# Kernel tuning notes

Hardware: AMD Instinct MI355X
Metric: run time of the kernel (lower is better)

## Reference

```python
import jax, jax.numpy as jnp
import numpy as np

N_SITES = 64   # lattice sites
BOND = 32      # virtual bond dimension D
PHYS = 2       # physical (spin) dimension
BATCH = 32768  # Monte Carlo samples


def spin_to_occupancy(s):
    # spins in {-1,+1} -> physical indices in {0,1}
    return ((s + 1) // 2).astype(jnp.int32)


def setup_inputs() -> dict:
    key = jax.random.key(0)
    k1, k2, k3, k4 = jax.random.split(key, 4)
    # site tensors: boundary sites have bond dim 1, interior sites are (PHYS, D, D)
    t_first = jax.random.uniform(k1, (PHYS, 1, BOND), dtype=jnp.float32)
    t_mid = jax.random.uniform(k2, (N_SITES - 2, PHYS, BOND, BOND), dtype=jnp.float32)
    t_last = jax.random.uniform(k3, (PHYS, BOND, 1), dtype=jnp.float32)
    bits = jax.random.randint(k4, (BATCH, N_SITES), 0, 2)
    x = (2 * bits - 1).astype(jnp.int32)  # spins +-1
    return {"t_first": t_first, "t_mid": t_mid, "t_last": t_last, "x": x}


def reference(t_first, t_mid, t_last, x):
    idx = spin_to_occupancy(x)  # (B, n_sites)
    # first site: left bond = 1, so state = t_first[idx0, 0, :]  (B, D)
    state = t_first[idx[:, 0], 0, :]

    # interior sites: sequential chain of gather + batched mat-vec
    def step(state, xs):
        T, i = xs            # T: (PHYS, D, D), i: (B,)
        mats = T[i]          # (B, D, D) gather by physical index
        return jnp.einsum('bi,bij->bj', state, mats), None

    state, _ = jax.lax.scan(step, state, (t_mid, idx[:, 1:-1].T))

    # last site: right bond = 1
    amps = jnp.einsum('bi,bi->b', state, t_last[idx[:, -1], :, 0])  # (B,)
    return jnp.log(amps)
```

## Files before the change

kernel.cpp:

```cpp
#include <hip/hip_runtime.h>
#include <math.h>

#define N_MID 62
#define NPAIR 31
#define BATCH 32768

typedef float f32x4 __attribute__((ext_vector_type(4)));
typedef unsigned int u32x2 __attribute__((ext_vector_type(2)));
typedef unsigned int u32x4 __attribute__((ext_vector_type(4)));

__device__ __forceinline__ long mklong(unsigned a, unsigned b) {
    u32x2 t = {a, b};
    return __builtin_bit_cast(long, t);
}
__device__ __forceinline__ unsigned pack_fp8x4(float a, float b, float c, float d) {
    int r = __builtin_amdgcn_cvt_pk_fp8_f32(a, b, 0, false);
    r = __builtin_amdgcn_cvt_pk_fp8_f32(c, d, r, true);
    return (unsigned)r;
}

__global__ __launch_bounds__(64) void prefix_kernel(const float* __restrict__ t_mid,
                                                    unsigned* __restrict__ wsP) {
    __shared__ float M1s[1024], M2s[1024];
    const int l = threadIdx.x, q = l >> 4, m = l & 15;
    const int i = blockIdx.x >> 2, v = blockIdx.x & 3;

    const float4* s1 = (const float4*)(t_mid + (size_t)((2 * i) * 2 + (v & 1)) * 1024);
    const float4* s2 = (const float4*)(t_mid + (size_t)((2 * i + 1) * 2 + (v >> 1)) * 1024);
    #pragma unroll
    for (int c = 0; c < 4; ++c) {
        ((float4*)M1s)[c * 64 + l] = s1[c * 64 + l];
        ((float4*)M2s)[c * 64 + l] = s2[c * 64 + l];
    }
    __syncthreads();

    float colv[2][32];
    #pragma unroll
    for (int t = 0; t < 2; ++t)
        #pragma unroll
        for (int mm = 0; mm < 32; ++mm)
            colv[t][mm] = M2s[mm * 32 + 16 * t + m];

    float o0[8], o1[8];
    #pragma unroll
    for (int j = 0; j < 8; ++j) {
        int a = 16 * (j >> 2) + 4 * q + (j & 3);
        float acc0 = 0.f, acc1 = 0.f;
        #pragma unroll
        for (int mm = 0; mm < 32; ++mm) {
            float r = M1s[a * 32 + mm];
            acc0 = fmaf(r, colv[0][mm], acc0);
            acc1 = fmaf(r, colv[1][mm], acc1);
        }
        o0[j] = acc0;
        o1[j] = acc1;
    }

    u32x4 outw;
    outw[0] = pack_fp8x4(o0[0], o0[1], o0[2], o0[3]);
    outw[1] = pack_fp8x4(o0[4], o0[5], o0[6], o0[7]);
    outw[2] = pack_fp8x4(o1[0], o1[1], o1[2], o1[3]);
    outw[3] = pack_fp8x4(o1[4], o1[5], o1[6], o1[7]);
    ((u32x4*)wsP)[blockIdx.x * 64 + l] = outw;
}

__global__ __launch_bounds__(256, 2) void mps_mfma_kernel(
    const float* __restrict__ t_first,
    const float* __restrict__ t_last,
    const int*   __restrict__ x,
    const unsigned* __restrict__ wsP,
    float* __restrict__ out)
{
    const int tid  = threadIdx.x;
    const int w    = tid >> 6;
    const int l    = tid & 63;
    const int q    = l >> 4;
    const int e    = l & 15;
    const int base = (blockIdx.x * 4 + w) * 16;

    unsigned long long mrot;
    {
        const int4* xr = (const int4*)(x + (size_t)(base + e) * 64 + 16 * q);
        unsigned chunk = 0;
        #pragma unroll
        for (int c = 0; c < 4; ++c) {
            int4 vv = xr[c];
            chunk |= (unsigned)(vv.x > 0) << (4 * c + 0);
            chunk |= (unsigned)(vv.y > 0) << (4 * c + 1);
            chunk |= (unsigned)(vv.z > 0) << (4 * c + 2);
            chunk |= (unsigned)(vv.w > 0) << (4 * c + 3);
        }
        unsigned sh = chunk << ((q & 1) * 16);
        unsigned lo = (q < 2) ? sh : 0u;
        unsigned hi = (q >= 2) ? sh : 0u;
        lo |= (unsigned)__shfl_xor((int)lo, 16);
        lo |= (unsigned)__shfl_xor((int)lo, 32);
        hi |= (unsigned)__shfl_xor((int)hi, 16);
        hi |= (unsigned)__shfl_xor((int)hi, 32);
        unsigned long long mask = ((unsigned long long)hi << 32) | lo;
        const float* tf = t_first + ((mask & 1ull) ? 32 : 0);
        mrot = mask >> 1;
        (void)tf;
    }

    float st[8];
    {
        const float* tf = t_first + ((x[(size_t)(base + e) * 64] > 0) ? 32 : 0);
        #pragma unroll
        for (int j = 0; j < 8; ++j)
            st[j] = tf[16 * (j >> 2) + 4 * q + (j & 3)];
    }
    unsigned Bd0 = pack_fp8x4(st[0], st[1], st[2], st[3]);
    unsigned Bd1 = pack_fp8x4(st[4], st[5], st[6], st[7]);

    int expsum = 0;
    const f32x4 cz = {0.f, 0.f, 0.f, 0.f};

    const u32x4* W = (const u32x4*)wsP + l;
    u32x4 Q0[4], Q1[4];
    #pragma unroll
    for (int v = 0; v < 4; ++v) Q0[v] = W[v * 64];
    #pragma unroll
    for (int v = 0; v < 4; ++v) Q1[v] = W[(4 + v) * 64];

    auto step = [&](u32x4* Q, const u32x4* pf) {
        unsigned vl = (unsigned)mrot & 3u;
        mrot >>= 2;

        f32x4 y0 = cz, y1 = cz;
        #pragma unroll
        for (int v = 0; v < 4; ++v) {
            long A0 = mklong(Q[v][0], Q[v][1]);
            long A1 = mklong(Q[v][2], Q[v][3]);
            bool sel = (vl == (unsigned)v);
            long u = mklong(sel ? Bd0 : 0u, sel ? Bd1 : 0u);
            y0 = __builtin_amdgcn_mfma_f32_16x16x32_fp8_fp8(A0, u, y0, 0, 0, 0);
            y1 = __builtin_amdgcn_mfma_f32_16x16x32_fp8_fp8(A1, u, y1, 0, 0, 0);
        }

        if (pf) {
            #pragma unroll
            for (int v = 0; v < 4; ++v) Q[v] = pf[v * 64];
        }

        #pragma unroll
        for (int r = 0; r < 4; ++r) { st[r] = y0[r]; st[4 + r] = y1[r]; }

        float mx = st[0];
        #pragma unroll
        for (int j = 1; j < 8; ++j) mx = fmaxf(mx, st[j]);
        mx = fmaxf(mx, __shfl_xor(mx, 16));
        mx = fmaxf(mx, __shfl_xor(mx, 32));
        int ex = (int)((__float_as_uint(mx) >> 23) & 0xFF) - 127;
        float sc = __uint_as_float((unsigned)(127 - ex) << 23);
        #pragma unroll
        for (int j = 0; j < 8; ++j) st[j] *= sc;
        expsum += ex;

        Bd0 = pack_fp8x4(st[0], st[1], st[2], st[3]);
        Bd1 = pack_fp8x4(st[4], st[5], st[6], st[7]);
    };

    const u32x4* pf = W + 8 * 64;
    for (int k = 0; k < 15; ++k) {
        step(Q0, pf);
        step(Q1, (k < 14) ? pf + 4 * 64 : nullptr);
        pf += 8 * 64;
    }
    step(Q0, nullptr);

    const float* tl = t_last + ((mrot & 1ull) ? 32 : 0);
    float amp = 0.f;
    #pragma unroll
    for (int j = 0; j < 8; ++j)
        amp = fmaf(st[j], tl[16 * (j >> 2) + 4 * q + (j & 3)], amp);
    amp += __shfl_xor(amp, 16);
    amp += __shfl_xor(amp, 32);

    if (l < 16)
        out[base + l] = logf(amp) + 0.69314718055994531f * (float)expsum;
}

extern "C" void kernel_launch(void* const* d_in, const int* in_sizes, int n_in,
                              void* d_out, int out_size, void* d_ws, size_t ws_size,
                              hipStream_t stream) {
    const float* t_first = (const float*)d_in[0];
    const float* t_mid   = (const float*)d_in[1];
    const float* t_last  = (const float*)d_in[2];
    const int*   x       = (const int*)d_in[3];
    float* out           = (float*)d_out;

    unsigned* wsP = (unsigned*)d_ws;

    hipLaunchKernelGGL(prefix_kernel, dim3(NPAIR * 4), dim3(64), 0, stream, t_mid, wsP);
    hipLaunchKernelGGL(mps_mfma_kernel, dim3(BATCH / 64), dim3(256), 0, stream,
                       t_first, t_last, x, wsP, out);
}
```

Baseline: 77.70 us.

## Split MPS chain into forward and backward halves meeting in the middle

The chain contraction is split so that even waves contract left-to-right from the first site and odd waves contract right-to-left from the last site. The two halves meet through shared memory for the final dot product. Each wave now processes two 16-sample groups, interleaving their independent MFMA chains. This halves the sequential dependency length and adds instruction-level parallelism, at the cost of more registers, a block-wide barrier, and a reworked prefix kernel that builds backward-transposed pair products.

Result: slower. 82.73 us (+6.5%).

```diff
diff --git a/kernel.cpp b/kernel.cpp
--- a/kernel.cpp
+++ b/kernel.cpp
@@ -1,8 +1,6 @@
 #include <hip/hip_runtime.h>
 #include <math.h>
 
-#define N_MID 62
-#define NPAIR 31
 #define BATCH 32768
 
 typedef float f32x4 __attribute__((ext_vector_type(4)));
@@ -18,42 +16,76 @@
     r = __builtin_amdgcn_cvt_pk_fp8_f32(c, d, r, true);
     return (unsigned)r;
 }
+__device__ __forceinline__ int lamf(int q, int j) { return 16 * (j >> 2) + 4 * q + (j & 3); }
 
 __global__ __launch_bounds__(64) void prefix_kernel(const float* __restrict__ t_mid,
                                                     unsigned* __restrict__ wsP) {
     __shared__ float M1s[1024], M2s[1024];
     const int l = threadIdx.x, q = l >> 4, m = l & 15;
-    const int i = blockIdx.x >> 2, v = blockIdx.x & 3;
-
-    const float4* s1 = (const float4*)(t_mid + (size_t)((2 * i) * 2 + (v & 1)) * 1024);
-    const float4* s2 = (const float4*)(t_mid + (size_t)((2 * i + 1) * 2 + (v >> 1)) * 1024);
-    #pragma unroll
-    for (int c = 0; c < 4; ++c) {
-        ((float4*)M1s)[c * 64 + l] = s1[c * 64 + l];
-        ((float4*)M2s)[c * 64 + l] = s2[c * 64 + l];
-    }
-    __syncthreads();
-
-    float colv[2][32];
-    #pragma unroll
-    for (int t = 0; t < 2; ++t)
-        #pragma unroll
-        for (int mm = 0; mm < 32; ++mm)
-            colv[t][mm] = M2s[mm * 32 + 16 * t + m];
+    const int bi = blockIdx.x;
+
+    bool fwd, pair;
+    int v, m1i = 0, m2i = 0;
+    if (bi < 2)       { fwd = true;  pair = false; v = bi;            m1i = 0; }
+    else if (bi < 62) { fwd = true;  pair = true;  v = (bi - 2) & 3;  int i = (bi - 2) >> 2;  m1i = 2 * i + 1; m2i = 2 * i + 2; }
+    else if (bi < 64) { fwd = false; pair = false; v = bi - 62;       m1i = 61; }
+    else              { fwd = false; pair = true;  v = (bi - 64) & 3; int i = (bi - 64) >> 2; m1i = 59 - 2 * i; m2i = 60 - 2 * i; }
 
     float o0[8], o1[8];
-    #pragma unroll
-    for (int j = 0; j < 8; ++j) {
-        int a = 16 * (j >> 2) + 4 * q + (j & 3);
-        float acc0 = 0.f, acc1 = 0.f;
-        #pragma unroll
-        for (int mm = 0; mm < 32; ++mm) {
-            float r = M1s[a * 32 + mm];
-            acc0 = fmaf(r, colv[0][mm], acc0);
-            acc1 = fmaf(r, colv[1][mm], acc1);
-        }
-        o0[j] = acc0;
-        o1[j] = acc1;
+    if (pair) {
+        const float4* s1 = (const float4*)(t_mid + (size_t)(m1i * 2 + (v & 1)) * 1024);
+        const float4* s2 = (const float4*)(t_mid + (size_t)(m2i * 2 + (v >> 1)) * 1024);
+        #pragma unroll
+        for (int c = 0; c < 4; ++c) {
+            ((float4*)M1s)[c * 64 + l] = s1[c * 64 + l];
+            ((float4*)M2s)[c * 64 + l] = s2[c * 64 + l];
+        }
+        __syncthreads();
+        if (fwd) {
+            float colv[2][32];
+            #pragma unroll
+            for (int t = 0; t < 2; ++t)
+                #pragma unroll
+                for (int c = 0; c < 32; ++c) colv[t][c] = M2s[c * 32 + 16 * t + m];
+            #pragma unroll
+            for (int j = 0; j < 8; ++j) {
+                int a = lamf(q, j);
+                float a0 = 0.f, a1 = 0.f;
+                #pragma unroll
+                for (int c = 0; c < 32; ++c) {
+                    float r = M1s[a * 32 + c];
+                    a0 = fmaf(r, colv[0][c], a0);
+                    a1 = fmaf(r, colv[1][c], a1);
+                }
+                o0[j] = a0; o1[j] = a1;
+            }
+        } else {
+            float rowv[2][32];
+            #pragma unroll
+            for (int t = 0; t < 2; ++t)
+                #pragma unroll
+                for (int c = 0; c < 32; ++c) rowv[t][c] = M1s[(16 * t + m) * 32 + c];
+            #pragma unroll
+            for (int j = 0; j < 8; ++j) {
+                int a = lamf(q, j);
+                float a0 = 0.f, a1 = 0.f;
+                #pragma unroll
+                for (int c = 0; c < 32; ++c) {
+                    float s = M2s[c * 32 + a];
+                    a0 = fmaf(rowv[0][c], s, a0);
+                    a1 = fmaf(rowv[1][c], s, a1);
+                }
+                o0[j] = a0; o1[j] = a1;
+            }
+        }
+    } else {
+        const float* T = t_mid + (size_t)(m1i * 2 + v) * 1024;
+        #pragma unroll
+        for (int j = 0; j < 8; ++j) {
+            int a = lamf(q, j);
+            if (fwd) { o0[j] = T[a * 32 + m];      o1[j] = T[a * 32 + 16 + m]; }
+            else     { o0[j] = T[m * 32 + a];      o1[j] = T[(16 + m) * 32 + a]; }
+        }
     }
 
     u32x4 outw;
@@ -61,7 +93,7 @@
     outw[1] = pack_fp8x4(o0[4], o0[5], o0[6], o0[7]);
     outw[2] = pack_fp8x4(o1[0], o1[1], o1[2], o1[3]);
     outw[3] = pack_fp8x4(o1[4], o1[5], o1[6], o1[7]);
-    ((u32x4*)wsP)[blockIdx.x * 64 + l] = outw;
+    ((u32x4*)wsP)[bi * 64 + l] = outw;
 }
 
 __global__ __launch_bounds__(256, 2) void mps_mfma_kernel(
@@ -71,16 +103,20 @@
     const unsigned* __restrict__ wsP,
     float* __restrict__ out)
 {
+    __shared__ float Lf[2][64][17];
+    __shared__ int   Le[2][32];
+
     const int tid  = threadIdx.x;
     const int w    = tid >> 6;
     const int l    = tid & 63;
     const int q    = l >> 4;
     const int e    = l & 15;
-    const int base = (blockIdx.x * 4 + w) * 16;
-
-    unsigned long long mrot;
-    {
-        const int4* xr = (const int4*)(x + (size_t)(base + e) * 64 + 16 * q);
+    const bool isf = (w & 1) == 0;
+    const int egrp = w >> 1;
+    const int base = blockIdx.x * 64 + egrp * 32;
+
+    auto build_mask = [&](int elem) -> unsigned long long {
+        const int4* xr = (const int4*)(x + (size_t)elem * 64 + 16 * q);
         unsigned chunk = 0;
         #pragma unroll
         for (int c = 0; c < 4; ++c) {
@@ -97,88 +133,124 @@
         lo |= (unsigned)__shfl_xor((int)lo, 32);
         hi |= (unsigned)__shfl_xor((int)hi, 16);
         hi |= (unsigned)__shfl_xor((int)hi, 32);
-        unsigned long long mask = ((unsigned long long)hi << 32) | lo;
-        const float* tf = t_first + ((mask & 1ull) ? 32 : 0);
-        mrot = mask >> 1;
-        (void)tf;
-    }
-
-    float st[8];
+        return ((unsigned long long)hi << 32) | lo;
+    };
+    const unsigned long long mA = build_mask(base + e);
+    const unsigned long long mB = build_mask(base + 16 + e);
+
+    float stA[8], stB[8];
     {
-        const float* tf = t_first + ((x[(size_t)(base + e) * 64] > 0) ? 32 : 0);
-        #pragma unroll
-        for (int j = 0; j < 8; ++j)
-            st[j] = tf[16 * (j >> 2) + 4 * q + (j & 3)];
-    }
-    unsigned Bd0 = pack_fp8x4(st[0], st[1], st[2], st[3]);
-    unsigned Bd1 = pack_fp8x4(st[4], st[5], st[6], st[7]);
-
-    int expsum = 0;
+        const float* pa;
+        const float* pb;
+        if (isf) {
+            pa = t_first + ((mA & 1ull) ? 32 : 0);
+            pb = t_first + ((mB & 1ull) ? 32 : 0);
+        } else {
+            pa = t_last + (((mA >> 63) & 1ull) ? 32 : 0);
+            pb = t_last + (((mB >> 63) & 1ull) ? 32 : 0);
+        }
+        #pragma unroll
+        for (int j = 0; j < 8; ++j) {
+            int c = lamf(q, j);
+            stA[j] = pa[c];
+            stB[j] = pb[c];
+        }
+    }
+    unsigned BdA0 = pack_fp8x4(stA[0], stA[1], stA[2], stA[3]);
+    unsigned BdA1 = pack_fp8x4(stA[4], stA[5], stA[6], stA[7]);
+    unsigned BdB0 = pack_fp8x4(stB[0], stB[1], stB[2], stB[3]);
+    unsigned BdB1 = pack_fp8x4(stB[4], stB[5], stB[6], stB[7]);
+
+    int expA = 0, expB = 0;
     const f32x4 cz = {0.f, 0.f, 0.f, 0.f};
-
-    const u32x4* W = (const u32x4*)wsP + l;
-    u32x4 Q0[4], Q1[4];
+    const u32x4* W = (const u32x4*)wsP + l + (isf ? 0 : 62 * 64);
+
+    u32x4 Qs[2];
+    Qs[0] = W[0]; Qs[1] = W[64];
+    u32x4 Q[2][4];
     #pragma unroll
-    for (int v = 0; v < 4; ++v) Q0[v] = W[v * 64];
+    for (int v = 0; v < 4; ++v) { Q[0][v] = W[(2 + v) * 64]; Q[1][v] = W[(6 + v) * 64]; }
+
+    auto dostep = [&](u32x4* Qv, int nvar, unsigned vlA, unsigned vlB,
+                      const u32x4* pf) {
+        f32x4 yA0 = cz, yA1 = cz, yB0 = cz, yB1 = cz;
+        #pragma unroll
+        for (int v = 0; v < 4; ++v) {
+            if (v >= nvar) break;
+            long A0 = mklong(Qv[v][0], Qv[v][1]);
+            long A1 = mklong(Qv[v][2], Qv[v][3]);
+            bool sA = (vlA == (unsigned)v);
+            bool sB = (vlB == (unsigned)v);
+            long uA = mklong(sA ? BdA0 : 0u, sA ? BdA1 : 0u);
+            long uB = mklong(sB ? BdB0 : 0u, sB ? BdB1 : 0u);
+            yA0 = __builtin_amdgcn_mfma_f32_16x16x32_fp8_fp8(A0, uA, yA0, 0, 0, 0);
+            yA1 = __builtin_amdgcn_mfma_f32_16x16x32_fp8_fp8(A1, uA, yA1, 0, 0, 0);
+            yB0 = __builtin_amdgcn_mfma_f32_16x16x32_fp8_fp8(A0, uB, yB0, 0, 0, 0);
+            yB1 = __builtin_amdgcn_mfma_f32_16x16x32_fp8_fp8(A1, uB, yB1, 0, 0, 0);
+        }
+        if (pf) {
+            #pragma unroll
+            for (int v = 0; v < 4; ++v) Qv[v] = pf[v * 64];
+        }
+        #pragma unroll
+        for (int r = 0; r < 4; ++r) {
+            stA[r] = yA0[r]; stA[4 + r] = yA1[r];
+            stB[r] = yB0[r]; stB[4 + r] = yB1[r];
+        }
+        float mxA = stA[0], mxB = stB[0];
+        #pragma unroll
+        for (int j = 1; j < 8; ++j) { mxA = fmaxf(mxA, stA[j]); mxB = fmaxf(mxB, stB[j]); }
+        mxA = fmaxf(mxA, __shfl_xor(mxA, 16)); mxA = fmaxf(mxA, __shfl_xor(mxA, 32));
+        mxB = fmaxf(mxB, __shfl_xor(mxB, 16)); mxB = fmaxf(mxB, __shfl_xor(mxB, 32));
+        int exA = (int)((__float_as_uint(mxA) >> 23) & 0xFF) - 127;
+        int exB = (int)((__float_as_uint(mxB) >> 23) & 0xFF) - 127;
+        float scA = __uint_as_float((unsigned)(127 - exA) << 23);
+        float scB = __uint_as_float((unsigned)(127 - exB) << 23);
+        #pragma unroll
+        for (int j = 0; j < 8; ++j) { stA[j] *= scA; stB[j] *= scB; }
+        expA += exA; expB += exB;
+        BdA0 = pack_fp8x4(stA[0], stA[1], stA[2], stA[3]);
+        BdA1 = pack_fp8x4(stA[4], stA[5], stA[6], stA[7]);
+        BdB0 = pack_fp8x4(stB[0], stB[1], stB[2], stB[3]);
+        BdB1 = pack_fp8x4(stB[4], stB[5], stB[6], stB[7]);
+    };
+
+    {
+        int ss = isf ? 1 : 62;
+        dostep(Qs, 2, (unsigned)((mA >> ss) & 1ull), (unsigned)((mB >> ss) & 1ull), nullptr);
+    }
     #pragma unroll
-    for (int v = 0; v < 4; ++v) Q1[v] = W[(4 + v) * 64];
-
-    auto step = [&](u32x4* Q, const u32x4* pf) {
-        unsigned vl = (unsigned)mrot & 3u;
-        mrot >>= 2;
-
-        f32x4 y0 = cz, y1 = cz;
-        #pragma unroll
-        for (int v = 0; v < 4; ++v) {
-            long A0 = mklong(Q[v][0], Q[v][1]);
-            long A1 = mklong(Q[v][2], Q[v][3]);
-            bool sel = (vl == (unsigned)v);
-            long u = mklong(sel ? Bd0 : 0u, sel ? Bd1 : 0u);
-            y0 = __builtin_amdgcn_mfma_f32_16x16x32_fp8_fp8(A0, u, y0, 0, 0, 0);
-            y1 = __builtin_amdgcn_mfma_f32_16x16x32_fp8_fp8(A1, u, y1, 0, 0, 0);
-        }
-
-        if (pf) {
-            #pragma unroll
-            for (int v = 0; v < 4; ++v) Q[v] = pf[v * 64];
-        }
-
-        #pragma unroll
-        for (int r = 0; r < 4; ++r) { st[r] = y0[r]; st[4 + r] = y1[r]; }
-
-        float mx = st[0];
-        #pragma unroll
-        for (int j = 1; j < 8; ++j) mx = fmaxf(mx, st[j]);
-        mx = fmaxf(mx, __shfl_xor(mx, 16));
-        mx = fmaxf(mx, __shfl_xor(mx, 32));
-        int ex = (int)((__float_as_uint(mx) >> 23) & 0xFF) - 127;
-        float sc = __uint_as_float((unsigned)(127 - ex) << 23);
-        #pragma unroll
-        for (int j = 0; j < 8; ++j) st[j] *= sc;
-        expsum += ex;
-
-        Bd0 = pack_fp8x4(st[0], st[1], st[2], st[3]);
-        Bd1 = pack_fp8x4(st[4], st[5], st[6], st[7]);
-    };
-
-    const u32x4* pf = W + 8 * 64;
     for (int k = 0; k < 15; ++k) {
-        step(Q0, pf);
-        step(Q1, (k < 14) ? pf + 4 * 64 : nullptr);
-        pf += 8 * 64;
-    }
-    step(Q0, nullptr);
-
-    const float* tl = t_last + ((mrot & 1ull) ? 32 : 0);
-    float amp = 0.f;
-    #pragma unroll
-    for (int j = 0; j < 8; ++j)
-        amp = fmaf(st[j], tl[16 * (j >> 2) + 4 * q + (j & 3)], amp);
-    amp += __shfl_xor(amp, 16);
-    amp += __shfl_xor(amp, 32);
-
-    if (l < 16)
-        out[base + l] = logf(amp) + 0.69314718055994531f * (float)expsum;
+        int sh = isf ? (2 + 2 * k) : (60 - 2 * k);
+        unsigned vA = (unsigned)((mA >> sh) & 3ull);
+        unsigned vB = (unsigned)((mB >> sh) & 3ull);
+        const u32x4* pf = (k < 13) ? (W + (size_t)(2 + 4 * (k + 2)) * 64) : nullptr;
+        dostep(Q[k & 1], 4, vA, vB, pf);
+    }
+
+    if (isf) {
+        #pragma unroll
+        for (int j = 0; j < 8; ++j) {
+            Lf[egrp][l][j]     = stA[j];
+            Lf[egrp][l][8 + j] = stB[j];
+        }
+        if (q == 0) { Le[egrp][e] = expA; Le[egrp][16 + e] = expB; }
+    }
+    __syncthreads();
+    if (!isf) {
+        float ampA = 0.f, ampB = 0.f;
+        #pragma unroll
+        for (int j = 0; j < 8; ++j) {
+            ampA = fmaf(Lf[egrp][l][j],     stA[j], ampA);
+            ampB = fmaf(Lf[egrp][l][8 + j], stB[j], ampB);
+        }
+        ampA += __shfl_xor(ampA, 16); ampA += __shfl_xor(ampA, 32);
+        ampB += __shfl_xor(ampB, 16); ampB += __shfl_xor(ampB, 32);
+        if (l < 16) {
+            out[base + l]      = logf(ampA) + 0.69314718055994531f * (float)(Le[egrp][l] + expA);
+            out[base + 16 + l] = logf(ampB) + 0.69314718055994531f * (float)(Le[egrp][16 + l] + expB);
+        }
+    }
 }
 
 extern "C" void kernel_launch(void* const* d_in, const int* in_sizes, int n_in,
@@ -192,7 +264,7 @@
 
     unsigned* wsP = (unsigned*)d_ws;
 
-    hipLaunchKernelGGL(prefix_kernel, dim3(NPAIR * 4), dim3(64), 0, stream, t_mid, wsP);
+    hipLaunchKernelGGL(prefix_kernel, dim3(124), dim3(64), 0, stream, t_mid, wsP);
     hipLaunchKernelGGL(mps_mfma_kernel, dim3(BATCH / 64), dim3(256), 0, stream,
                        t_first, t_last, x, wsP, out);
 }
```

## Stage precomputed fp8 pair-products in LDS and double block size

Applied to the files above, without the earlier changes.

The main kernel now copies the whole precomputed fp8 pair-product table (about 127 KB) into shared memory once per block. The per-step prefetches then read from LDS instead of global/L2 memory. Blocks grow from 256 to 512 threads to amortize the copy, and the first-site lookup reuses the packed spin mask instead of a separate global load. The large LDS footprint limits occupancy to one block per CU and adds an upfront copy plus a barrier before the chain starts.

After: 82.69 us. 1.06x slower.

```diff
diff --git a/kernel.cpp b/kernel.cpp
--- a/kernel.cpp
+++ b/kernel.cpp
@@ -4,6 +4,7 @@
 #define N_MID 62
 #define NPAIR 31
 #define BATCH 32768
+#define NCHUNK (NPAIR * 4 * 64)
 
 typedef float f32x4 __attribute__((ext_vector_type(4)));
 typedef unsigned int u32x2 __attribute__((ext_vector_type(2)));
@@ -64,21 +65,29 @@
     ((u32x4*)wsP)[blockIdx.x * 64 + l] = outw;
 }
 
-__global__ __launch_bounds__(256, 2) void mps_mfma_kernel(
+__global__ __launch_bounds__(512, 2) void mps_mfma_kernel(
     const float* __restrict__ t_first,
     const float* __restrict__ t_last,
     const int*   __restrict__ x,
     const unsigned* __restrict__ wsP,
     float* __restrict__ out)
 {
+    __shared__ u32x4 LP[NCHUNK];
+
     const int tid  = threadIdx.x;
     const int w    = tid >> 6;
     const int l    = tid & 63;
     const int q    = l >> 4;
     const int e    = l & 15;
-    const int base = (blockIdx.x * 4 + w) * 16;
-
-    unsigned long long mrot;
+    const int base = (blockIdx.x * 8 + w) * 16;
+
+    {
+        const u32x4* src = (const u32x4*)wsP;
+        for (int i = tid; i < NCHUNK; i += 512)
+            LP[i] = src[i];
+    }
+
+    unsigned long long mask;
     {
         const int4* xr = (const int4*)(x + (size_t)(base + e) * 64 + 16 * q);
         unsigned chunk = 0;
@@ -97,33 +106,32 @@
         lo |= (unsigned)__shfl_xor((int)lo, 32);
         hi |= (unsigned)__shfl_xor((int)hi, 16);
         hi |= (unsigned)__shfl_xor((int)hi, 32);
-        unsigned long long mask = ((unsigned long long)hi << 32) | lo;
-        const float* tf = t_first + ((mask & 1ull) ? 32 : 0);
-        mrot = mask >> 1;
-        (void)tf;
+        mask = ((unsigned long long)hi << 32) | lo;
     }
 
     float st[8];
     {
-        const float* tf = t_first + ((x[(size_t)(base + e) * 64] > 0) ? 32 : 0);
+        const float* tf = t_first + ((mask & 1ull) ? 32 : 0);
         #pragma unroll
         for (int j = 0; j < 8; ++j)
             st[j] = tf[16 * (j >> 2) + 4 * q + (j & 3)];
     }
+    unsigned long long mrot = mask >> 1;
     unsigned Bd0 = pack_fp8x4(st[0], st[1], st[2], st[3]);
     unsigned Bd1 = pack_fp8x4(st[4], st[5], st[6], st[7]);
 
     int expsum = 0;
     const f32x4 cz = {0.f, 0.f, 0.f, 0.f};
 
-    const u32x4* W = (const u32x4*)wsP + l;
+    __syncthreads();
+
     u32x4 Q0[4], Q1[4];
     #pragma unroll
-    for (int v = 0; v < 4; ++v) Q0[v] = W[v * 64];
-    #pragma unroll
-    for (int v = 0; v < 4; ++v) Q1[v] = W[(4 + v) * 64];
-
-    auto step = [&](u32x4* Q, const u32x4* pf) {
+    for (int v = 0; v < 4; ++v) Q0[v] = LP[v * 64 + l];
+    #pragma unroll
+    for (int v = 0; v < 4; ++v) Q1[v] = LP[(4 + v) * 64 + l];
+
+    auto step = [&](u32x4* Q, int pfIdx) {
         unsigned vl = (unsigned)mrot & 3u;
         mrot >>= 2;
 
@@ -138,9 +146,9 @@
             y1 = __builtin_amdgcn_mfma_f32_16x16x32_fp8_fp8(A1, u, y1, 0, 0, 0);
         }
 
-        if (pf) {
+        if (pfIdx >= 0) {
             #pragma unroll
-            for (int v = 0; v < 4; ++v) Q[v] = pf[v * 64];
+            for (int v = 0; v < 4; ++v) Q[v] = LP[pfIdx + v * 64 + l];
         }
 
         #pragma unroll
@@ -161,13 +169,11 @@
         Bd1 = pack_fp8x4(st[4], st[5], st[6], st[7]);
     };
 
-    const u32x4* pf = W + 8 * 64;
     for (int k = 0; k < 15; ++k) {
-        step(Q0, pf);
-        step(Q1, (k < 14) ? pf + 4 * 64 : nullptr);
-        pf += 8 * 64;
-    }
-    step(Q0, nullptr);
+        step(Q0, (2 * k + 2) * 256);
+        step(Q1, (k < 14) ? (2 * k + 3) * 256 : -1);
+    }
+    step(Q0, -1);
 
     const float* tl = t_last + ((mrot & 1ull) ? 32 : 0);
     float amp = 0.f;
@@ -193,6 +199,6 @@
     unsigned* wsP = (unsigned*)d_ws;
 
     hipLaunchKernelGGL(prefix_kernel, dim3(NPAIR * 4), dim3(64), 0, stream, t_mid, wsP);
-    hipLaunchKernelGGL(mps_mfma_kernel, dim3(BATCH / 64), dim3(256), 0, stream,
+    hipLaunchKernelGGL(mps_mfma_kernel, dim3(BATCH / 128), dim3(512), 0, stream,
                        t_first, t_last, x, wsP, out);
 }
```
